# Optimization experiments

Hardware: AMD Instinct MI355X
Metric: run time of the kernel (lower is better)

The kernel has to match this reference:

```python
import jax, jax.numpy as jnp
import numpy as np

D_MODEL = 1024
HEADS = 16
D_K = D_MODEL // HEADS
B, S = 2, 2048
NEG = -1000000000.0

def setup_inputs() -> dict:
    key = jax.random.key(0)
    ks = jax.random.split(key, 11)
    sc = 1.0 / np.sqrt(D_MODEL)
    inp = {
        'q': jax.random.normal(ks[0], (B, S, D_MODEL), jnp.float32),
        'k': jax.random.normal(ks[1], (B, S, D_MODEL), jnp.float32),
        'v': jax.random.normal(ks[2], (B, S, D_MODEL), jnp.float32),
        'mask': jnp.tril(jnp.ones((S, S), jnp.int32))[None, None],  # causal [1,1,S,S]
        'wq_w': jax.random.normal(ks[3], (D_MODEL, D_MODEL), jnp.float32) * sc,
        'wq_b': jax.random.normal(ks[4], (D_MODEL,), jnp.float32) * 0.02,
        'wk_w': jax.random.normal(ks[5], (D_MODEL, D_MODEL), jnp.float32) * sc,
        'wk_b': jax.random.normal(ks[6], (D_MODEL,), jnp.float32) * 0.02,
        'wv_w': jax.random.normal(ks[7], (D_MODEL, D_MODEL), jnp.float32) * sc,
        'wv_b': jax.random.normal(ks[8], (D_MODEL,), jnp.float32) * 0.02,
        'wo_w': jax.random.normal(ks[9], (D_MODEL, D_MODEL), jnp.float32) * sc,
        'wo_b': jax.random.normal(ks[10], (D_MODEL,), jnp.float32) * 0.02,
    }
    return inp

def reference(q, k, v, mask, wq_w, wq_b, wk_w, wk_b, wv_w, wv_b, wo_w, wo_b):
    b, s, _ = q.shape
    # projections (torch Linear: x @ W^T + b)
    Q = (q @ wq_w.T + wq_b).reshape(b, s, HEADS, D_K).transpose(0, 2, 1, 3)  # [B,H,S,Dk]
    K = (k @ wk_w.T + wk_b).reshape(b, s, HEADS, D_K).transpose(0, 2, 1, 3)
    V = (v @ wv_w.T + wv_b).reshape(b, s, HEADS, D_K).transpose(0, 2, 1, 3)
    scores = jnp.einsum('bhqd,bhkd->bhqk', Q, K) / jnp.sqrt(jnp.float32(D_K))
    scores = jnp.where(mask == 0, NEG, scores)
    p = jax.nn.softmax(scores, axis=-1)  # dropout=0.0 -> identity
    x = jnp.einsum('bhqk,bhkd->bhqd', p, V)
    x = x.transpose(0, 2, 1, 3).reshape(b, s, D_MODEL)
    return x @ wo_w.T + wo_b
```

## Files before the change

kernel.cpp:

```cpp
#include <hip/hip_runtime.h>

typedef unsigned short u16;
typedef __attribute__((ext_vector_type(8))) short bf16x8;
typedef __attribute__((ext_vector_type(4))) float f32x4;

#define SEQ 2048
#define DMODEL 1024

__device__ __forceinline__ u16 f2bf(float f) {
    union { float f; unsigned u; } x; x.f = f;
    unsigned r = x.u + 0x7fffu + ((x.u >> 16) & 1u);
    return (u16)(r >> 16);
}

__device__ __forceinline__ u16 f2bf_trunc(float f) {
    union { float f; unsigned u; } x; x.f = f;
    return (u16)(x.u >> 16);
}

__device__ __forceinline__ float bf2f(u16 v) {
    union { unsigned u; float f; } x; x.u = ((unsigned)v) << 16;
    return x.f;
}

__device__ __forceinline__ f32x4 mfma16(bf16x8 a, bf16x8 b, f32x4 c) {
    return __builtin_amdgcn_mfma_f32_16x16x32_bf16(a, b, c, 0, 0, 0);
}

__device__ __forceinline__ void gld16(const u16* g, u16* l) {
    __builtin_amdgcn_global_load_lds(
        (__attribute__((address_space(1))) const void*)g,
        (__attribute__((address_space(3))) void*)l, 16, 0, 0);
}

struct CvtArgs {
    const float* src[7];
    u16* dst[7];
    int n4[7];
};

__global__ __launch_bounds__(256) void cvt_kernel(CvtArgs a) {
    const int id = blockIdx.y;
    const int i = blockIdx.x * 256 + threadIdx.x;
    if (i >= a.n4[id]) return;
    float4 f = ((const float4*)a.src[id])[i];
    ushort4 u;
    u.x = f2bf(f.x); u.y = f2bf(f.y); u.z = f2bf(f.z); u.w = f2bf(f.w);
    ((ushort4*)a.dst[id])[i] = u;
}


__global__ __launch_bounds__(512, 2) void gemm_qkv(
    const u16* __restrict__ Xq, const u16* __restrict__ Xk, const u16* __restrict__ Xv,
    const u16* __restrict__ Wq, const u16* __restrict__ Wk, const u16* __restrict__ Wv,
    const float* __restrict__ bq, const float* __restrict__ bk, const float* __restrict__ bv,
    u16* __restrict__ Qb, u16* __restrict__ Kb, u16* __restrict__ Vb)
{
    __shared__ u16 Abuf[2][256 * 64];
    __shared__ u16 Bbuf[2][256 * 64];

    const int bid = blockIdx.x;
    const int G = (bid & 7) * 24 + (bid >> 3);
    const int z = G >> 6;
    const int rem = G & 63;
    const int bm = (rem >> 2) * 256;
    const int bn = (rem & 3) * 256;

    const u16* X = (z == 0) ? Xq : (z == 1) ? Xk : Xv;
    const u16* W = (z == 0) ? Wq : (z == 1) ? Wk : Wv;
    const float* bias = (z == 0) ? bq : (z == 1) ? bk : bv;

    const int tid = threadIdx.x;
    const int lane = tid & 63, w = tid >> 6;
    const int wr = w >> 2, wc = w & 3;
    const int r = lane & 15, qd = lane >> 4;

    const int srow = lane >> 3;
    const int scol = ((lane & 7) ^ srow) * 8;
    const u16* Xs = X + (size_t)(bm + w * 32 + srow) * 1024 + scol;
    const u16* Ws = W + (size_t)(bn + w * 32 + srow) * 1024 + scol;

    const int rxor = (r & 7) << 4;
    const int rowA = (wr * 128 + r) * 128;
    const int rowB = (wc * 64 + r) * 128;
    const int ko0 = (qd * 16) ^ rxor;
    const int ko1 = (64 + qd * 16) ^ rxor;

    f32x4 acc[8][4];
    #pragma unroll
    for (int i = 0; i < 8; ++i)
        #pragma unroll
        for (int j = 0; j < 4; ++j)
            acc[i][j] = (f32x4){0.f, 0.f, 0.f, 0.f};

    auto stage = [&](int t) {
        const int d = t & 1;
        const u16* xa = Xs + t * 64;
        const u16* wb = Ws + t * 64;
        u16* Al = &Abuf[d][w * 2048];
        u16* Bl = &Bbuf[d][w * 2048];
        #pragma unroll
        for (int q = 0; q < 4; ++q) {
            gld16(xa + (size_t)q * 8192, Al + q * 512);
            gld16(wb + (size_t)q * 8192, Bl + q * 512);
        }
    };

    stage(0);
    stage(1);
    asm volatile("s_waitcnt vmcnt(8)" ::: "memory");
    __builtin_amdgcn_sched_barrier(0);
    __builtin_amdgcn_s_barrier();

    for (int t = 0; t < 16; ++t) {
        const u16* Ab = Abuf[t & 1];
        const u16* Bb = Bbuf[t & 1];
        #pragma unroll
        for (int kc = 0; kc < 2; ++kc) {
            const int ko = kc ? ko1 : ko0;
            bf16x8 aF[8], bF[4];
            #pragma unroll
            for (int m = 0; m < 8; ++m)
                aF[m] = *(const bf16x8*)((const char*)Ab + rowA + m * 2048 + ko);
            #pragma unroll
            for (int n = 0; n < 4; ++n)
                bF[n] = *(const bf16x8*)((const char*)Bb + rowB + n * 2048 + ko);
            __builtin_amdgcn_s_setprio(1);
            #pragma unroll
            for (int m = 0; m < 8; ++m)
                #pragma unroll
                for (int n = 0; n < 4; ++n)
                    acc[m][n] = mfma16(aF[m], bF[n], acc[m][n]);
            __builtin_amdgcn_s_setprio(0);
        }
        if (t == 15) break;
        asm volatile("s_waitcnt lgkmcnt(0)" ::: "memory");
        __builtin_amdgcn_sched_barrier(0);
        __builtin_amdgcn_s_barrier();
        if (t < 14) {
            stage(t + 2);
            asm volatile("s_waitcnt vmcnt(8)" ::: "memory");
        } else {
            asm volatile("s_waitcnt vmcnt(0)" ::: "memory");
        }
        __builtin_amdgcn_sched_barrier(0);
        __builtin_amdgcn_s_barrier();
        __builtin_amdgcn_sched_barrier(0);
    }

    const float scale = (z == 0) ? 0.125f : 1.0f;
    #pragma unroll
    for (int j = 0; j < 4; ++j) {
        const int n = bn + wc * 64 + j * 16 + r;
        const float bvl = bias[n];
        const int h = n >> 6, d = n & 63;
        #pragma unroll
        for (int i = 0; i < 8; ++i) {
            const int m0 = bm + wr * 128 + i * 16 + qd * 4;
            const int b_ = m0 >> 11, s0 = m0 & 2047;
            if (z == 0) {
                #pragma unroll
                for (int reg = 0; reg < 4; ++reg)
                    Qb[(size_t)(m0 + reg) * 1024 + n] = f2bf((acc[i][j][reg] + bvl) * scale);
            } else if (z == 1) {
                #pragma unroll
                for (int reg = 0; reg < 4; ++reg)
                    Kb[((size_t)(b_ * 16 + h) * SEQ + s0 + reg) * 64 + d] =
                        f2bf(acc[i][j][reg] + bvl);
            } else {
                ushort4 u;
                u.x = f2bf(acc[i][j][0] + bvl);
                u.y = f2bf(acc[i][j][1] + bvl);
                u.z = f2bf(acc[i][j][2] + bvl);
                u.w = f2bf(acc[i][j][3] + bvl);
                *(ushort4*)(Vb + ((size_t)(b_ * 16 + h) * 64 + d) * SEQ + s0) = u;
            }
        }
    }
}

__global__ __launch_bounds__(256, 3) void attn_kernel(
    const u16* __restrict__ Qb, const u16* __restrict__ Kb,
    const u16* __restrict__ Vb, u16* __restrict__ Op, float* __restrict__ Lp)
{
    __shared__ u16 Kst[2][4096];
    __shared__ u16 Vst[2][4096];
    __shared__ u16 Pst[4][16 * 72];

    const int bid = blockIdx.x;
    const int xcd = bid & 7;
    const int i2 = bid >> 3;
    const int bh = xcd + 8 * (i2 & 3);
    const int rest = i2 >> 2;
    const int gidx = rest / 3;
    const int third = rest - gidx * 3;
    const int g = 31 - gidx;
    const int b_ = bh >> 4, h = bh & 15;

    const int n = g + 1;
    const int j0 = (n * third) / 3;
    const int j1 = (n * (third + 1)) / 3;

    const int tid = threadIdx.x;
    const int lane = tid & 63, w = tid >> 6;
    const int r = lane & 15, qd = lane >> 4;

    const u16* Kh = Kb + (size_t)bh * SEQ * 64;
    const u16* Vh = Vb + (size_t)bh * 64 * SEQ;
    u16* Pw = Pst[w];

    bf16x8 aQ[2];
    {
        const size_t qoff =
            (size_t)(b_ * SEQ + g * 64 + w * 16 + r) * DMODEL + h * 64;
        aQ[0] = *(const bf16x8*)(Qb + qoff + qd * 8);
        aQ[1] = *(const bf16x8*)(Qb + qoff + 32 + qd * 8);
    }

    bf16x8 ones;
    #pragma unroll
    for (int e = 0; e < 8; ++e) ones[e] = (short)0x3F80;

    f32x4 o[4];
    f32x4 l = (f32x4){0.f, 0.f, 0.f, 0.f};
    #pragma unroll
    for (int db = 0; db < 4; ++db) o[db] = (f32x4){0.f, 0.f, 0.f, 0.f};

    auto stage = [&](int j, int buf) {
        if (w < 2) {
            const u16* Kt = Kh + (size_t)j * 64 * 64;
            #pragma unroll
            for (int s = 0; s < 4; ++s) {
                const int ss = w * 4 + s;
                gld16(Kt + ((ss >> 1) * 16 + r) * 64 + (ss & 1) * 32 + qd * 8,
                      &Kst[buf][ss * 512]);
            }
        } else {
            const u16* Vt = Vh + j * 64;
            #pragma unroll
            for (int s = 0; s < 4; ++s) {
                const int ss = (w - 2) * 4 + s;
                gld16(Vt + (size_t)((ss >> 1) * 16 + r) * SEQ + (ss & 1) * 32 + qd * 8,
                      &Vst[buf][ss * 512]);
            }
        }
    };

    if (j0 < j1) stage(j0, j0 & 1);

    for (int j = j0; j < j1; ++j) {
        const int cur = j & 1;
        __syncthreads();
        if (j + 1 < j1) stage(j + 1, 1 - cur);

        bf16x8 kf[4][2], vf[4][2];
        #pragma unroll
        for (int nb = 0; nb < 4; ++nb) {
            kf[nb][0] = *(const bf16x8*)(&Kst[cur][(nb * 2 + 0) * 512 + lane * 8]);
            kf[nb][1] = *(const bf16x8*)(&Kst[cur][(nb * 2 + 1) * 512 + lane * 8]);
        }
        #pragma unroll
        for (int db = 0; db < 4; ++db) {
            vf[db][0] = *(const bf16x8*)(&Vst[cur][(db * 2 + 0) * 512 + lane * 8]);
            vf[db][1] = *(const bf16x8*)(&Vst[cur][(db * 2 + 1) * 512 + lane * 8]);
        }

        f32x4 sc[4];
        #pragma unroll
        for (int nb = 0; nb < 4; ++nb) {
            f32x4 s = (f32x4){0.f, 0.f, 0.f, 0.f};
            s = mfma16(kf[nb][0], aQ[0], s);
            s = mfma16(kf[nb][1], aQ[1], s);
            sc[nb] = s;
        }

        if (j == g) {
            const int rowr = w * 16 + r;
            #pragma unroll
            for (int nb = 0; nb < 4; ++nb)
                #pragma unroll
                for (int reg = 0; reg < 4; ++reg)
                    if (nb * 16 + qd * 4 + reg > rowr) sc[nb][reg] = -1e30f;
        }

        #pragma unroll
        for (int nb = 0; nb < 4; ++nb)
            #pragma unroll
            for (int reg = 0; reg < 4; ++reg)
                sc[nb][reg] = exp2f(fmaf(sc[nb][reg], 1.4426950408889634f,
                                         -23.083120654223414f));

        #pragma unroll
        for (int nb = 0; nb < 4; ++nb) {
            ushort4 pk;
            pk.x = f2bf_trunc(sc[nb][0]);
            pk.y = f2bf_trunc(sc[nb][1]);
            pk.z = f2bf_trunc(sc[nb][2]);
            pk.w = f2bf_trunc(sc[nb][3]);
            *(ushort4*)(Pw + r * 72 + nb * 16 + qd * 4) = pk;
        }

        const bf16x8 aP0 = *(const bf16x8*)(Pw + r * 72 + qd * 8);
        const bf16x8 aP1 = *(const bf16x8*)(Pw + r * 72 + 32 + qd * 8);

        l = mfma16(aP0, ones, l);
        l = mfma16(aP1, ones, l);

        #pragma unroll
        for (int db = 0; db < 4; ++db) {
            o[db] = mfma16(aP0, vf[db][0], o[db]);
            o[db] = mfma16(aP1, vf[db][1], o[db]);
        }
    }

    u16* Oh = Op + ((size_t)(third * 1024 + bh * 32 + g) * 4096);
    float* Lh = Lp + (size_t)(third * 1024 + bh * 32 + g) * 64;
    #pragma unroll
    for (int db = 0; db < 4; ++db)
        #pragma unroll
        for (int reg = 0; reg < 4; ++reg)
            Oh[(w * 16 + qd * 4 + reg) * 64 + db * 16 + r] = f2bf(o[db][reg]);
    if (r == 0) {
        #pragma unroll
        for (int reg = 0; reg < 4; ++reg)
            Lh[w * 16 + qd * 4 + reg] = l[reg];
    }
}

__global__ __launch_bounds__(256) void attn_norm(
    const u16* __restrict__ Op, const float* __restrict__ Lp,
    u16* __restrict__ AO)
{
    const int idx = blockIdx.x * 256 + threadIdx.x;
    const int col8 = idx & 127;
    const int row = idx >> 7;
    const int h = col8 >> 3;
    const int b_ = row >> 11, s = row & 2047;
    const int g = s >> 6, r64 = s & 63;
    const int bh = b_ * 16 + h;

    const size_t pa = ((size_t)(bh * 32 + g) * 4096) + r64 * 64 + (col8 & 7) * 8;
    const size_t pb = pa + (size_t)1024 * 4096;
    const size_t pc = pb + (size_t)1024 * 4096;
    const float la = Lp[(bh * 32 + g) * 64 + r64];
    const float lb = Lp[(1024 + bh * 32 + g) * 64 + r64];
    const float lc = Lp[(2048 + bh * 32 + g) * 64 + r64];
    const float inv = 1.0f / (la + lb + lc);

    const bf16x8 a = *(const bf16x8*)(Op + pa);
    const bf16x8 b = *(const bf16x8*)(Op + pb);
    const bf16x8 c = *(const bf16x8*)(Op + pc);
    bf16x8 o;
    #pragma unroll
    for (int e = 0; e < 8; ++e)
        o[e] = (short)f2bf((bf2f((u16)a[e]) + bf2f((u16)b[e]) + bf2f((u16)c[e])) * inv);
    *(bf16x8*)(AO + (size_t)row * 1024 + col8 * 8) = o;
}

__global__ __launch_bounds__(512, 2) void gemm_out(
    const u16* __restrict__ AO, const u16* __restrict__ W,
    const float* __restrict__ bias, float* __restrict__ out)
{
    __shared__ u16 Abuf[2][256 * 64];
    __shared__ u16 Bbuf[2][256 * 64];

    const int bid = blockIdx.x;
    const int G = (bid & 7) * 8 + (bid >> 3);
    const int bm = (G >> 2) * 256;
    const int bn = (G & 3) * 256;

    const int tid = threadIdx.x;
    const int lane = tid & 63, w = tid >> 6;
    const int wr = w >> 2, wc = w & 3;
    const int r = lane & 15, qd = lane >> 4;

    const int srow = lane >> 3;
    const int scol = ((lane & 7) ^ srow) * 8;
    const u16* Xs = AO + (size_t)(bm + w * 32 + srow) * 1024 + scol;
    const u16* Ws = W + (size_t)(bn + w * 32 + srow) * 1024 + scol;

    const int rxor = (r & 7) << 4;
    const int rowA = (wr * 128 + r) * 128;
    const int rowB = (wc * 64 + r) * 128;
    const int ko0 = (qd * 16) ^ rxor;
    const int ko1 = (64 + qd * 16) ^ rxor;

    f32x4 acc[8][4];
    #pragma unroll
    for (int i = 0; i < 8; ++i)
        #pragma unroll
        for (int j = 0; j < 4; ++j)
            acc[i][j] = (f32x4){0.f, 0.f, 0.f, 0.f};

    auto stage = [&](int t) {
        const int d = t & 1;
        const u16* xa = Xs + t * 64;
        const u16* wb = Ws + t * 64;
        u16* Al = &Abuf[d][w * 2048];
        u16* Bl = &Bbuf[d][w * 2048];
        #pragma unroll
        for (int q = 0; q < 4; ++q) {
            gld16(xa + (size_t)q * 8192, Al + q * 512);
            gld16(wb + (size_t)q * 8192, Bl + q * 512);
        }
    };

    stage(0);
    stage(1);
    asm volatile("s_waitcnt vmcnt(8)" ::: "memory");
    __builtin_amdgcn_sched_barrier(0);
    __builtin_amdgcn_s_barrier();

    for (int t = 0; t < 16; ++t) {
        const u16* Ab = Abuf[t & 1];
        const u16* Bb = Bbuf[t & 1];
        #pragma unroll
        for (int kc = 0; kc < 2; ++kc) {
            const int ko = kc ? ko1 : ko0;
            bf16x8 aF[8], bF[4];
            #pragma unroll
            for (int m = 0; m < 8; ++m)
                aF[m] = *(const bf16x8*)((const char*)Ab + rowA + m * 2048 + ko);
            #pragma unroll
            for (int n = 0; n < 4; ++n)
                bF[n] = *(const bf16x8*)((const char*)Bb + rowB + n * 2048 + ko);
            __builtin_amdgcn_s_setprio(1);
            #pragma unroll
            for (int m = 0; m < 8; ++m)
                #pragma unroll
                for (int n = 0; n < 4; ++n)
                    acc[m][n] = mfma16(aF[m], bF[n], acc[m][n]);
            __builtin_amdgcn_s_setprio(0);
        }
        if (t == 15) break;
        asm volatile("s_waitcnt lgkmcnt(0)" ::: "memory");
        __builtin_amdgcn_sched_barrier(0);
        __builtin_amdgcn_s_barrier();
        if (t < 14) {
            stage(t + 2);
            asm volatile("s_waitcnt vmcnt(8)" ::: "memory");
        } else {
            asm volatile("s_waitcnt vmcnt(0)" ::: "memory");
        }
        __builtin_amdgcn_sched_barrier(0);
        __builtin_amdgcn_s_barrier();
        __builtin_amdgcn_sched_barrier(0);
    }

    #pragma unroll
    for (int j = 0; j < 4; ++j) {
        const int n = bn + wc * 64 + j * 16 + r;
        const float bvl = bias[n];
        #pragma unroll
        for (int i = 0; i < 8; ++i) {
            const int m0 = bm + wr * 128 + i * 16 + qd * 4;
            #pragma unroll
            for (int reg = 0; reg < 4; ++reg)
                out[(size_t)(m0 + reg) * 1024 + n] = acc[i][j][reg] + bvl;
        }
    }
}

extern "C" void kernel_launch(void* const* d_in, const int* in_sizes, int n_in,
                              void* d_out, int out_size, void* d_ws, size_t ws_size,
                              hipStream_t stream) {
    const float* q  = (const float*)d_in[0];
    const float* k  = (const float*)d_in[1];
    const float* v  = (const float*)d_in[2];
    const float* wq = (const float*)d_in[4];
    const float* bq = (const float*)d_in[5];
    const float* wk = (const float*)d_in[6];
    const float* bk = (const float*)d_in[7];
    const float* wv = (const float*)d_in[8];
    const float* bv = (const float*)d_in[9];
    const float* wo = (const float*)d_in[10];
    const float* bo = (const float*)d_in[11];
    float* out = (float*)d_out;

    u16* ws = (u16*)d_ws;
    u16* Xq = ws;
    u16* Xk = Xq + (size_t)4194304;
    u16* Xv = Xk + (size_t)4194304;
    u16* Wq = Xv + (size_t)4194304;
    u16* Wk = Wq + (size_t)1048576;
    u16* Wv = Wk + (size_t)1048576;
    u16* Wo = Wv + (size_t)1048576;
    u16* Qb = Wo + (size_t)1048576;
    u16* Kb = Qb + (size_t)4194304;
    u16* Vb = Kb + (size_t)4194304;
    u16* AO = Vb + (size_t)4194304;

    u16* Op = ws;
    float* Lp = (float*)(ws + (size_t)12582912);

    CvtArgs ca;
    ca.src[0] = q;  ca.dst[0] = Xq; ca.n4[0] = 1048576;
    ca.src[1] = k;  ca.dst[1] = Xk; ca.n4[1] = 1048576;
    ca.src[2] = v;  ca.dst[2] = Xv; ca.n4[2] = 1048576;
    ca.src[3] = wq; ca.dst[3] = Wq; ca.n4[3] = 262144;
    ca.src[4] = wk; ca.dst[4] = Wk; ca.n4[4] = 262144;
    ca.src[5] = wv; ca.dst[5] = Wv; ca.n4[5] = 262144;
    ca.src[6] = wo; ca.dst[6] = Wo; ca.n4[6] = 262144;

    cvt_kernel<<<dim3(4096, 7), 256, 0, stream>>>(ca);
    gemm_qkv<<<dim3(192), 512, 0, stream>>>(Xq, Xk, Xv, Wq, Wk, Wv,
                                            bq, bk, bv, Qb, Kb, Vb);
    attn_kernel<<<dim3(3072), 256, 0, stream>>>(Qb, Kb, Vb, Op, Lp);
    attn_norm<<<dim3(2048), 256, 0, stream>>>(Op, Lp, AO);
    gemm_out<<<dim3(64), 512, 0, stream>>>(AO, Wo, bo, out);
}
```

Measured before the change: 256.4 us.

## Shrink GEMM tiles for more blocks and fold softmax scale into Q

```diff
diff --git a/kernel.cpp b/kernel.cpp
--- a/kernel.cpp
+++ b/kernel.cpp
@@ -50,21 +50,21 @@
 }
 
 
-__global__ __launch_bounds__(512, 2) void gemm_qkv(
+__global__ __launch_bounds__(256, 4) void gemm_qkv(
     const u16* __restrict__ Xq, const u16* __restrict__ Xk, const u16* __restrict__ Xv,
     const u16* __restrict__ Wq, const u16* __restrict__ Wk, const u16* __restrict__ Wv,
     const float* __restrict__ bq, const float* __restrict__ bk, const float* __restrict__ bv,
     u16* __restrict__ Qb, u16* __restrict__ Kb, u16* __restrict__ Vb)
 {
-    __shared__ u16 Abuf[2][256 * 64];
-    __shared__ u16 Bbuf[2][256 * 64];
+    __shared__ u16 Abuf[2][128 * 32];
+    __shared__ u16 Bbuf[2][128 * 32];
 
     const int bid = blockIdx.x;
-    const int G = (bid & 7) * 24 + (bid >> 3);
-    const int z = G >> 6;
-    const int rem = G & 63;
-    const int bm = (rem >> 2) * 256;
-    const int bn = (rem & 3) * 256;
+    const int gm = (bid & 7) * 96 + (bid >> 3);
+    const int z = gm >> 8;
+    const int rem = gm & 255;
+    const int bm = (rem >> 3) * 128;
+    const int bn = (rem & 7) * 128;
 
     const u16* X = (z == 0) ? Xq : (z == 1) ? Xk : Xv;
     const u16* W = (z == 0) ? Wq : (z == 1) ? Wk : Wv;
@@ -72,74 +72,60 @@
 
     const int tid = threadIdx.x;
     const int lane = tid & 63, w = tid >> 6;
-    const int wr = w >> 2, wc = w & 3;
+    const int wm = (w >> 1) * 64, wn = (w & 1) * 64;
     const int r = lane & 15, qd = lane >> 4;
 
-    const int srow = lane >> 3;
-    const int scol = ((lane & 7) ^ srow) * 8;
+    const int srow = lane >> 2;
+    const int scol = (lane & 3) * 8;
     const u16* Xs = X + (size_t)(bm + w * 32 + srow) * 1024 + scol;
     const u16* Ws = W + (size_t)(bn + w * 32 + srow) * 1024 + scol;
 
-    const int rxor = (r & 7) << 4;
-    const int rowA = (wr * 128 + r) * 128;
-    const int rowB = (wc * 64 + r) * 128;
-    const int ko0 = (qd * 16) ^ rxor;
-    const int ko1 = (64 + qd * 16) ^ rxor;
-
-    f32x4 acc[8][4];
-    #pragma unroll
-    for (int i = 0; i < 8; ++i)
+    f32x4 acc[4][4];
+    #pragma unroll
+    for (int i = 0; i < 4; ++i)
         #pragma unroll
         for (int j = 0; j < 4; ++j)
             acc[i][j] = (f32x4){0.f, 0.f, 0.f, 0.f};
 
     auto stage = [&](int t) {
         const int d = t & 1;
-        const u16* xa = Xs + t * 64;
-        const u16* wb = Ws + t * 64;
-        u16* Al = &Abuf[d][w * 2048];
-        u16* Bl = &Bbuf[d][w * 2048];
-        #pragma unroll
-        for (int q = 0; q < 4; ++q) {
-            gld16(xa + (size_t)q * 8192, Al + q * 512);
-            gld16(wb + (size_t)q * 8192, Bl + q * 512);
+        #pragma unroll
+        for (int q = 0; q < 2; ++q) {
+            gld16(Xs + (size_t)q * 16384 + t * 32, &Abuf[d][w * 1024 + q * 512]);
+            gld16(Ws + (size_t)q * 16384 + t * 32, &Bbuf[d][w * 1024 + q * 512]);
         }
     };
 
     stage(0);
     stage(1);
-    asm volatile("s_waitcnt vmcnt(8)" ::: "memory");
+    asm volatile("s_waitcnt vmcnt(4)" ::: "memory");
     __builtin_amdgcn_sched_barrier(0);
     __builtin_amdgcn_s_barrier();
 
-    for (int t = 0; t < 16; ++t) {
+    for (int t = 0; t < 32; ++t) {
         const u16* Ab = Abuf[t & 1];
         const u16* Bb = Bbuf[t & 1];
-        #pragma unroll
-        for (int kc = 0; kc < 2; ++kc) {
-            const int ko = kc ? ko1 : ko0;
-            bf16x8 aF[8], bF[4];
-            #pragma unroll
-            for (int m = 0; m < 8; ++m)
-                aF[m] = *(const bf16x8*)((const char*)Ab + rowA + m * 2048 + ko);
-            #pragma unroll
-            for (int n = 0; n < 4; ++n)
-                bF[n] = *(const bf16x8*)((const char*)Bb + rowB + n * 2048 + ko);
-            __builtin_amdgcn_s_setprio(1);
-            #pragma unroll
-            for (int m = 0; m < 8; ++m)
-                #pragma unroll
-                for (int n = 0; n < 4; ++n)
-                    acc[m][n] = mfma16(aF[m], bF[n], acc[m][n]);
-            __builtin_amdgcn_s_setprio(0);
-        }
-        if (t == 15) break;
+        bf16x8 aF[4], bF[4];
+        #pragma unroll
+        for (int i = 0; i < 4; ++i)
+            aF[i] = *(const bf16x8*)(Ab + (wm + i * 16 + r) * 32 + qd * 8);
+        #pragma unroll
+        for (int j = 0; j < 4; ++j)
+            bF[j] = *(const bf16x8*)(Bb + (wn + j * 16 + r) * 32 + qd * 8);
+        __builtin_amdgcn_s_setprio(1);
+        #pragma unroll
+        for (int i = 0; i < 4; ++i)
+            #pragma unroll
+            for (int j = 0; j < 4; ++j)
+                acc[i][j] = mfma16(aF[i], bF[j], acc[i][j]);
+        __builtin_amdgcn_s_setprio(0);
+        if (t == 31) break;
         asm volatile("s_waitcnt lgkmcnt(0)" ::: "memory");
         __builtin_amdgcn_sched_barrier(0);
         __builtin_amdgcn_s_barrier();
-        if (t < 14) {
+        if (t < 30) {
             stage(t + 2);
-            asm volatile("s_waitcnt vmcnt(8)" ::: "memory");
+            asm volatile("s_waitcnt vmcnt(4)" ::: "memory");
         } else {
             asm volatile("s_waitcnt vmcnt(0)" ::: "memory");
         }
@@ -148,15 +134,15 @@
         __builtin_amdgcn_sched_barrier(0);
     }
 
-    const float scale = (z == 0) ? 0.125f : 1.0f;
+    const float scale = (z == 0) ? 0.18033688011112042f : 1.0f;
     #pragma unroll
     for (int j = 0; j < 4; ++j) {
-        const int n = bn + wc * 64 + j * 16 + r;
+        const int n = bn + wn + j * 16 + r;
         const float bvl = bias[n];
         const int h = n >> 6, d = n & 63;
         #pragma unroll
-        for (int i = 0; i < 8; ++i) {
-            const int m0 = bm + wr * 128 + i * 16 + qd * 4;
+        for (int i = 0; i < 4; ++i) {
+            const int m0 = bm + wm + i * 16 + qd * 4;
             const int b_ = m0 >> 11, s0 = m0 & 2047;
             if (z == 0) {
                 #pragma unroll
@@ -248,6 +234,9 @@
 
     if (j0 < j1) stage(j0, j0 & 1);
 
+    const f32x4 shift = (f32x4){-23.083120654223414f, -23.083120654223414f,
+                                -23.083120654223414f, -23.083120654223414f};
+
     for (int j = j0; j < j1; ++j) {
         const int cur = j & 1;
         __syncthreads();
@@ -268,7 +257,7 @@
         f32x4 sc[4];
         #pragma unroll
         for (int nb = 0; nb < 4; ++nb) {
-            f32x4 s = (f32x4){0.f, 0.f, 0.f, 0.f};
+            f32x4 s = shift;
             s = mfma16(kf[nb][0], aQ[0], s);
             s = mfma16(kf[nb][1], aQ[1], s);
             sc[nb] = s;
@@ -287,8 +276,7 @@
         for (int nb = 0; nb < 4; ++nb)
             #pragma unroll
             for (int reg = 0; reg < 4; ++reg)
-                sc[nb][reg] = exp2f(fmaf(sc[nb][reg], 1.4426950408889634f,
-                                         -23.083120654223414f));
+                sc[nb][reg] = exp2f(sc[nb][reg]);
 
         #pragma unroll
         for (int nb = 0; nb < 4; ++nb) {
@@ -357,88 +345,73 @@
     *(bf16x8*)(AO + (size_t)row * 1024 + col8 * 8) = o;
 }
 
-__global__ __launch_bounds__(512, 2) void gemm_out(
+__global__ __launch_bounds__(256, 4) void gemm_out(
     const u16* __restrict__ AO, const u16* __restrict__ W,
     const float* __restrict__ bias, float* __restrict__ out)
 {
-    __shared__ u16 Abuf[2][256 * 64];
-    __shared__ u16 Bbuf[2][256 * 64];
+    __shared__ u16 Abuf[2][64 * 32];
+    __shared__ u16 Bbuf[2][128 * 32];
 
     const int bid = blockIdx.x;
-    const int G = (bid & 7) * 8 + (bid >> 3);
-    const int bm = (G >> 2) * 256;
-    const int bn = (G & 3) * 256;
+    const int gm = (bid & 7) * 64 + (bid >> 3);
+    const int bm = (gm >> 3) * 64;
+    const int bn = (gm & 7) * 128;
 
     const int tid = threadIdx.x;
     const int lane = tid & 63, w = tid >> 6;
-    const int wr = w >> 2, wc = w & 3;
+    const int wm = (w >> 1) * 32, wn = (w & 1) * 64;
     const int r = lane & 15, qd = lane >> 4;
 
-    const int srow = lane >> 3;
-    const int scol = ((lane & 7) ^ srow) * 8;
-    const u16* Xs = AO + (size_t)(bm + w * 32 + srow) * 1024 + scol;
+    const int srow = lane >> 2;
+    const int scol = (lane & 3) * 8;
+    const u16* Xs = AO + (size_t)(bm + w * 16 + srow) * 1024 + scol;
     const u16* Ws = W + (size_t)(bn + w * 32 + srow) * 1024 + scol;
 
-    const int rxor = (r & 7) << 4;
-    const int rowA = (wr * 128 + r) * 128;
-    const int rowB = (wc * 64 + r) * 128;
-    const int ko0 = (qd * 16) ^ rxor;
-    const int ko1 = (64 + qd * 16) ^ rxor;
-
-    f32x4 acc[8][4];
-    #pragma unroll
-    for (int i = 0; i < 8; ++i)
+    f32x4 acc[2][4];
+    #pragma unroll
+    for (int i = 0; i < 2; ++i)
         #pragma unroll
         for (int j = 0; j < 4; ++j)
             acc[i][j] = (f32x4){0.f, 0.f, 0.f, 0.f};
 
     auto stage = [&](int t) {
         const int d = t & 1;
-        const u16* xa = Xs + t * 64;
-        const u16* wb = Ws + t * 64;
-        u16* Al = &Abuf[d][w * 2048];
-        u16* Bl = &Bbuf[d][w * 2048];
-        #pragma unroll
-        for (int q = 0; q < 4; ++q) {
-            gld16(xa + (size_t)q * 8192, Al + q * 512);
-            gld16(wb + (size_t)q * 8192, Bl + q * 512);
-        }
+        gld16(Xs + t * 32, &Abuf[d][w * 512]);
+        #pragma unroll
+        for (int q = 0; q < 2; ++q)
+            gld16(Ws + (size_t)q * 16384 + t * 32, &Bbuf[d][w * 1024 + q * 512]);
     };
 
     stage(0);
     stage(1);
-    asm volatile("s_waitcnt vmcnt(8)" ::: "memory");
+    asm volatile("s_waitcnt vmcnt(3)" ::: "memory");
     __builtin_amdgcn_sched_barrier(0);
     __builtin_amdgcn_s_barrier();
 
-    for (int t = 0; t < 16; ++t) {
+    for (int t = 0; t < 32; ++t) {
         const u16* Ab = Abuf[t & 1];
         const u16* Bb = Bbuf[t & 1];
-        #pragma unroll
-        for (int kc = 0; kc < 2; ++kc) {
-            const int ko = kc ? ko1 : ko0;
-            bf16x8 aF[8], bF[4];
-            #pragma unroll
-            for (int m = 0; m < 8; ++m)
-                aF[m] = *(const bf16x8*)((const char*)Ab + rowA + m * 2048 + ko);
-            #pragma unroll
-            for (int n = 0; n < 4; ++n)
-                bF[n] = *(const bf16x8*)((const char*)Bb + rowB + n * 2048 + ko);
-            __builtin_amdgcn_s_setprio(1);
-            #pragma unroll
-            for (int m = 0; m < 8; ++m)
-                #pragma unroll
-                for (int n = 0; n < 4; ++n)
-                    acc[m][n] = mfma16(aF[m], bF[n], acc[m][n]);
-            __builtin_amdgcn_s_setprio(0);
-        }
-        if (t == 15) break;
+        bf16x8 aF[2], bF[4];
+        #pragma unroll
+        for (int i = 0; i < 2; ++i)
+            aF[i] = *(const bf16x8*)(Ab + (wm + i * 16 + r) * 32 + qd * 8);
+        #pragma unroll
+        for (int j = 0; j < 4; ++j)
+            bF[j] = *(const bf16x8*)(Bb + (wn + j * 16 + r) * 32 + qd * 8);
+        __builtin_amdgcn_s_setprio(1);
+        #pragma unroll
+        for (int i = 0; i < 2; ++i)
+            #pragma unroll
+            for (int j = 0; j < 4; ++j)
+                acc[i][j] = mfma16(aF[i], bF[j], acc[i][j]);
+        __builtin_amdgcn_s_setprio(0);
+        if (t == 31) break;
         asm volatile("s_waitcnt lgkmcnt(0)" ::: "memory");
         __builtin_amdgcn_sched_barrier(0);
         __builtin_amdgcn_s_barrier();
-        if (t < 14) {
+        if (t < 30) {
             stage(t + 2);
-            asm volatile("s_waitcnt vmcnt(8)" ::: "memory");
+            asm volatile("s_waitcnt vmcnt(3)" ::: "memory");
         } else {
             asm volatile("s_waitcnt vmcnt(0)" ::: "memory");
         }
@@ -449,11 +422,11 @@
 
     #pragma unroll
     for (int j = 0; j < 4; ++j) {
-        const int n = bn + wc * 64 + j * 16 + r;
+        const int n = bn + wn + j * 16 + r;
         const float bvl = bias[n];
         #pragma unroll
-        for (int i = 0; i < 8; ++i) {
-            const int m0 = bm + wr * 128 + i * 16 + qd * 4;
+        for (int i = 0; i < 2; ++i) {
+            const int m0 = bm + wm + i * 16 + qd * 4;
             #pragma unroll
             for (int reg = 0; reg < 4; ++reg)
                 out[(size_t)(m0 + reg) * 1024 + n] = acc[i][j][reg] + bvl;
@@ -503,9 +476,9 @@
     ca.src[6] = wo; ca.dst[6] = Wo; ca.n4[6] = 262144;
 
     cvt_kernel<<<dim3(4096, 7), 256, 0, stream>>>(ca);
-    gemm_qkv<<<dim3(192), 512, 0, stream>>>(Xq, Xk, Xv, Wq, Wk, Wv,
+    gemm_qkv<<<dim3(768), 256, 0, stream>>>(Xq, Xk, Xv, Wq, Wk, Wv,
                                             bq, bk, bv, Qb, Kb, Vb);
     attn_kernel<<<dim3(3072), 256, 0, stream>>>(Qb, Kb, Vb, Op, Lp);
     attn_norm<<<dim3(2048), 256, 0, stream>>>(Op, Lp, AO);
-    gemm_out<<<dim3(64), 512, 0, stream>>>(AO, Wo, bo, out);
-}
+    gemm_out<<<dim3(512), 256, 0, stream>>>(AO, Wo, bo, out);
+}
```

New measurement: 234.3 us. 8.6% less time.
